# Performance work log

Hardware: AMD Instinct MI355X
Metric: run time of the kernel (lower is better)

The kernel has to match this reference:

```python
import jax, jax.numpy as jnp
import numpy as np

B, CIN, H, W = 4, 1024, 64, 64
PLANES = 256
K = 3
DIL = 2
PAD = DIL * (K - 1) // 2  # = 2
EPS = 1e-5


def setup_inputs() -> dict:
    key = jax.random.key(0)
    ks = jax.random.split(key, 16)
    d = {}
    d['x'] = jax.random.normal(ks[0], (B, CIN, H, W), dtype=jnp.float32)
    # conv1: 1x1, inplanes->planes, no bias
    d['w1'] = jax.random.normal(ks[1], (PLANES, CIN), dtype=jnp.float32) * 0.02
    d['gamma1'] = jnp.ones((PLANES,), jnp.float32)
    d['beta1'] = jnp.zeros((PLANES,), jnp.float32)
    d['mean1'] = jax.random.normal(ks[2], (PLANES,), dtype=jnp.float32) * 0.1
    d['var1'] = jax.random.uniform(ks[3], (PLANES,), minval=0.5, maxval=1.5, dtype=jnp.float32)
    # deform_offset: 3x3 conv planes->18, with bias
    d['woff'] = jax.random.normal(ks[4], (18, PLANES, K, K), dtype=jnp.float32) * 0.01
    d['boff'] = jnp.zeros((18,), jnp.float32)
    # conv2 (deformable): 3x3 planes->planes, with bias
    d['w2'] = jax.random.normal(ks[5], (PLANES, PLANES, K, K), dtype=jnp.float32) * 0.02
    d['bconv2'] = jnp.zeros((PLANES,), jnp.float32)
    d['gamma2'] = jnp.ones((PLANES,), jnp.float32)
    d['beta2'] = jnp.zeros((PLANES,), jnp.float32)
    d['mean2'] = jax.random.normal(ks[6], (PLANES,), dtype=jnp.float32) * 0.1
    d['var2'] = jax.random.uniform(ks[7], (PLANES,), minval=0.5, maxval=1.5, dtype=jnp.float32)
    # conv3: 1x1 planes->planes*4, no bias
    d['w3'] = jax.random.normal(ks[8], (PLANES * 4, PLANES), dtype=jnp.float32) * 0.02
    d['gamma3'] = jnp.ones((PLANES * 4,), jnp.float32)
    d['beta3'] = jnp.zeros((PLANES * 4,), jnp.float32)
    d['mean3'] = jax.random.normal(ks[9], (PLANES * 4,), dtype=jnp.float32) * 0.1
    d['var3'] = jax.random.uniform(ks[10], (PLANES * 4,), minval=0.5, maxval=1.5, dtype=jnp.float32)
    return d


def _bn(x, gamma, beta, mean, var):
    # inference-mode BatchNorm over channel dim (NCHW)
    inv = jax.lax.rsqrt(var + EPS)
    return (x - mean[:, None, None]) * (inv * gamma)[:, None, None] + beta[:, None, None]


def _deform_conv(x, offset, w, b):
    # x: [B,C,H,W]; offset: [B,18,H,W] ordered (dy,dx) per kernel tap; w: [O,C,3,3]
    Bn, C, Hh, Ww = x.shape
    off = offset.reshape(Bn, K * K, 2, Hh, Ww)
    off_y, off_x = off[:, :, 0], off[:, :, 1]          # [B,9,H,W]
    kk = jnp.arange(K * K)
    base_y = (kk // K) * DIL - PAD                      # [9]
    base_x = (kk % K) * DIL - PAD
    ys = jnp.arange(Hh, dtype=x.dtype)
    xs = jnp.arange(Ww, dtype=x.dtype)
    py = base_y.astype(x.dtype)[None, :, None, None] + ys[None, None, :, None] + off_y
    px = base_x.astype(x.dtype)[None, :, None, None] + xs[None, None, None, :] + off_x

    def sample_one(img, py1, px1):
        # img [C,H,W]; py1/px1 [9,H,W] -> [C,9,H,W] bilinear with zero padding
        y0 = jnp.floor(py1)
        x0 = jnp.floor(px1)
        wy = py1 - y0
        wx = px1 - x0

        def gather(yc, xc):
            yi = yc.astype(jnp.int32)
            xi = xc.astype(jnp.int32)
            valid = ((yi >= 0) & (yi < Hh) & (xi >= 0) & (xi < Ww)).astype(img.dtype)
            yi = jnp.clip(yi, 0, Hh - 1)
            xi = jnp.clip(xi, 0, Ww - 1)
            return img[:, yi, xi] * valid[None]

        v00 = gather(y0, x0)
        v01 = gather(y0, x0 + 1)
        v10 = gather(y0 + 1, x0)
        v11 = gather(y0 + 1, x0 + 1)
        return (v00 * ((1 - wy) * (1 - wx))[None] + v01 * ((1 - wy) * wx)[None]
                + v10 * (wy * (1 - wx))[None] + v11 * (wy * wx)[None])

    sampled = jax.vmap(sample_one)(x, py, px)           # [B,C,9,H,W]
    out = jnp.einsum('bckhw,ock->bohw', sampled, w.reshape(w.shape[0], C, K * K))
    return out + b[None, :, None, None]


def reference(x, w1, gamma1, beta1, mean1, var1, woff, boff, w2, bconv2,
              gamma2, beta2, mean2, var2, w3, gamma3, beta3, mean3, var3):
    residual = x
    out = jnp.einsum('bchw,oc->bohw', x, w1)            # conv1 1x1
    out = jax.nn.relu(_bn(out, gamma1, beta1, mean1, var1))
    offset = jax.lax.conv_general_dilated(
        out, woff, window_strides=(1, 1), padding=((PAD, PAD), (PAD, PAD)),
        rhs_dilation=(DIL, DIL), dimension_numbers=('NCHW', 'OIHW', 'NCHW'))
    offset = offset + boff[None, :, None, None]
    out = _deform_conv(out, offset, w2, bconv2)
    out = jax.nn.relu(_bn(out, gamma2, beta2, mean2, var2))
    out = jnp.einsum('bchw,oc->bohw', out, w3)          # conv3 1x1
    out = _bn(out, gamma3, beta3, mean3, var3)
    return jax.nn.relu(out + residual)
```

## Files before the change

### kernel.cpp

```cpp
#include <hip/hip_runtime.h>

#define EPS_BN 1e-5f

typedef __bf16 bf16x8 __attribute__((ext_vector_type(8)));
typedef float f32x4 __attribute__((ext_vector_type(4)));

__device__ __forceinline__ unsigned short f2bf(float f) {
  union { float f; unsigned u; } v; v.f = f;
  unsigned r = v.u + 0x7fffu + ((v.u >> 16) & 1u);
  return (unsigned short)(r >> 16);
}
__device__ __forceinline__ float bf2f(unsigned short h) {
  union { unsigned u; float f; } v; v.u = ((unsigned)h) << 16;
  return v.f;
}

__global__ __launch_bounds__(256) void prep_all(
    const float* __restrict__ w1, const float* __restrict__ w2, const float* __restrict__ woff,
    const float* __restrict__ w3,
    const float* g1, const float* b1, const float* m1, const float* v1,
    const float* g2, const float* b2, const float* m2, const float* v2, const float* bconv2,
    const float* g3, const float* b3, const float* m3, const float* v3,
    unsigned short* __restrict__ w1b, unsigned short* __restrict__ w2r,
    uint4* __restrict__ act1Pz, unsigned short* __restrict__ wob,
    unsigned short* __restrict__ w3b, float* __restrict__ shift3,
    float* s1, float* h1, float* s2, float* h2) {
  int bid = blockIdx.x, tid = threadIdx.x;
  if (bid < 1024) {
    int i = bid * 256 + tid;
    w1b[i] = f2bf(w1[i]);
  } else if (bid < 3328) {
    int i = (bid - 1024) * 256 + tid;
    int o = i / 2304, r = i % 2304;
    int kk = r / 256, c = r % 256;
    w2r[i] = f2bf(w2[(size_t)o * 2304 + c * 9 + kk]);
  } else if (bid < 5640) {
    int i = (bid - 3328) * 256 + tid;
    if (i < 591872) act1Pz[i] = uint4{0, 0, 0, 0};
  } else if (bid < 5928) {
    int i = (bid - 5640) * 256 + tid;
    int o = i / 2304, r = i % 2304;
    int kk = r / 256, c = r % 256;
    wob[i] = (o < 18) ? f2bf(woff[(size_t)o * 2304 + c * 9 + kk]) : (unsigned short)0;
  } else if (bid < 6952) {
    int i = (bid - 5928) * 256 + tid;
    int o = i >> 8;
    float sc = rsqrtf(v3[o] + EPS_BN) * g3[o];
    w3b[i] = f2bf(w3[i] * sc);
  } else if (bid < 6956) {
    int c = (bid - 6952) * 256 + tid;
    float sc = rsqrtf(v3[c] + EPS_BN) * g3[c];
    shift3[c] = b3[c] - m3[c] * sc;
  } else {
    int c = tid;
    float sc1 = rsqrtf(v1[c] + EPS_BN) * g1[c];
    s1[c] = sc1; h1[c] = b1[c] - m1[c] * sc1;
    float sc2 = rsqrtf(v2[c] + EPS_BN) * g2[c];
    s2[c] = sc2; h2[c] = b2[c] + (bconv2[c] - m2[c]) * sc2;
  }
}

__global__ __launch_bounds__(256) void transpose_x(const float* __restrict__ x,
                                                   unsigned short* __restrict__ xT) {
  __shared__ float t[32][33];
  int b = blockIdx.z;
  int p0 = blockIdx.x * 32, c0 = blockIdx.y * 32;
  int tx = threadIdx.x & 31, ty = threadIdx.x >> 5;
  const float* xb = x + (size_t)b * 1024 * 4096;
#pragma unroll
  for (int j = 0; j < 4; ++j) {
    int c = c0 + ty + j * 8;
    t[ty + j * 8][tx] = xb[(size_t)c * 4096 + p0 + tx];
  }
  __syncthreads();
  unsigned short* xTb = xT + (size_t)b * 4096 * 1024;
  int pl = threadIdx.x >> 3;
  int cl = (threadIdx.x & 7) * 4;
  float v0 = t[cl][pl], v1 = t[cl + 1][pl], v2 = t[cl + 2][pl], v3 = t[cl + 3][pl];
  uint2 pk;
  pk.x = (unsigned)f2bf(v0) | ((unsigned)f2bf(v1) << 16);
  pk.y = (unsigned)f2bf(v2) | ((unsigned)f2bf(v3) << 16);
  *(uint2*)(xTb + (size_t)(p0 + pl) * 1024 + c0 + cl) = pk;
}

__global__ __launch_bounds__(256) void gemm_split(
    const unsigned short* __restrict__ A, const unsigned short* __restrict__ Bm,
    unsigned short* __restrict__ part, int M, int N, int K, int KH) {
  __shared__ unsigned short sA[128 * 32];
  __shared__ unsigned short sB[128 * 32];
  __shared__ float tbuf[32 * 132];
  int tid = threadIdx.x, lane = tid & 63, wv = tid >> 6;
  int z = blockIdx.z;
  int m0 = blockIdx.y * 128, n0 = blockIdx.x * 128;
  f32x4 acc[4][4] = {};
  int rowA = tid >> 2;
  int kcol = (tid & 3) * 8;
  int wm = wv & 1, wn = wv >> 1;
  int lane15 = lane & 15, quad8 = (lane >> 4) * 8, quad = lane >> 4;
  int kend = z * KH + KH;

  for (int k0 = z * KH; k0 < kend; k0 += 32) {
    __syncthreads();
#pragma unroll
    for (int r = 0; r < 2; ++r) {
      const unsigned short* gp = A + (size_t)(m0 + r * 64 + rowA) * K + k0 + kcol;
      __builtin_amdgcn_global_load_lds((const __attribute__((address_space(1))) void*)gp,
                                       (__attribute__((address_space(3))) void*)&sA[r * 2048 + wv * 512],
                                       16, 0, 0);
    }
#pragma unroll
    for (int r = 0; r < 2; ++r) {
      const unsigned short* gp = Bm + (size_t)(n0 + r * 64 + rowA) * K + k0 + kcol;
      __builtin_amdgcn_global_load_lds((const __attribute__((address_space(1))) void*)gp,
                                       (__attribute__((address_space(3))) void*)&sB[r * 2048 + wv * 512],
                                       16, 0, 0);
    }
    __syncthreads();
    bf16x8 afr[4], bfr[4];
#pragma unroll
    for (int mi = 0; mi < 4; ++mi)
      afr[mi] = *(const bf16x8*)&sA[(wm * 64 + mi * 16 + lane15) * 32 + quad8];
#pragma unroll
    for (int ni = 0; ni < 4; ++ni)
      bfr[ni] = *(const bf16x8*)&sB[(wn * 64 + ni * 16 + lane15) * 32 + quad8];
#pragma unroll
    for (int mi = 0; mi < 4; ++mi)
#pragma unroll
      for (int ni = 0; ni < 4; ++ni)
        acc[mi][ni] = __builtin_amdgcn_mfma_f32_16x16x32_bf16(afr[mi], bfr[ni], acc[mi][ni], 0, 0, 0);
  }

  unsigned short* outH = part + (size_t)z * M * N;
  int trow = tid >> 3;
  int tcol16 = (tid & 7) * 16;
  int growBase = m0 + (trow >> 4) * 64 + (trow & 15);
#pragma unroll
  for (int mi = 0; mi < 4; ++mi) {
    __syncthreads();
#pragma unroll
    for (int ni = 0; ni < 4; ++ni)
#pragma unroll
      for (int reg = 0; reg < 4; ++reg)
        tbuf[(wm * 16 + quad * 4 + reg) * 132 + wn * 64 + ni * 16 + lane15] = acc[mi][ni][reg];
    __syncthreads();
    int gr = growBase + mi * 16;
    const float* lp = &tbuf[trow * 132 + tcol16];
    unsigned o[8];
#pragma unroll
    for (int j = 0; j < 8; ++j)
      o[j] = (unsigned)f2bf(lp[2 * j]) | ((unsigned)f2bf(lp[2 * j + 1]) << 16);
    unsigned short* op = outH + (size_t)gr * 256 + n0 + tcol16;
    *(uint4*)(op) = uint4{o[0], o[1], o[2], o[3]};
    *(uint4*)(op + 8) = uint4{o[4], o[5], o[6], o[7]};
  }
}

template <int NS, int PAD>
__global__ __launch_bounds__(256) void epi_bn(const unsigned short* __restrict__ part,
                                              const float* __restrict__ scale,
                                              const float* __restrict__ shift,
                                              unsigned short* __restrict__ outT,
                                              unsigned short* __restrict__ outP) {
  int gid = blockIdx.x * 256 + threadIdx.x;
  int row = gid >> 5, c0 = (gid & 31) * 8;
  float v[8] = {};
#pragma unroll
  for (int s = 0; s < NS; ++s) {
    uint4 q = *(const uint4*)(part + (size_t)s * 16384 * 256 + (size_t)row * 256 + c0);
    unsigned u[4] = {q.x, q.y, q.z, q.w};
#pragma unroll
    for (int j = 0; j < 4; ++j) {
      v[2 * j]     += bf2f((unsigned short)(u[j] & 0xffffu));
      v[2 * j + 1] += bf2f((unsigned short)(u[j] >> 16));
    }
  }
  float sc[8], sh[8];
  *(float4*)&sc[0] = *(const float4*)(scale + c0); *(float4*)&sc[4] = *(const float4*)(scale + c0 + 4);
  *(float4*)&sh[0] = *(const float4*)(shift + c0); *(float4*)&sh[4] = *(const float4*)(shift + c0 + 4);
  unsigned o[4];
#pragma unroll
  for (int j = 0; j < 4; ++j) {
    float lo = fmaxf(v[2 * j] * sc[2 * j] + sh[2 * j], 0.f);
    float hi = fmaxf(v[2 * j + 1] * sc[2 * j + 1] + sh[2 * j + 1], 0.f);
    o[j] = (unsigned)f2bf(lo) | ((unsigned)f2bf(hi) << 16);
  }
  uint4 pk{o[0], o[1], o[2], o[3]};
  *(uint4*)(outT + (size_t)row * 256 + c0) = pk;
  if constexpr (PAD) {
    int bb = row >> 12, p = row & 4095;
    *(uint4*)(outP + (((size_t)(bb * 68) + (p >> 6) + 2) * 68 + (p & 63) + 2) * 256 + c0) = pk;
  }
}

__global__ __launch_bounds__(256) void gemm_res(
    const unsigned short* __restrict__ A, const unsigned short* __restrict__ Bm,
    float* __restrict__ outp, const float* __restrict__ shift3,
    const float* __restrict__ resid, int M, int N, int K, long bStrideB, long bStrideOut) {
  __shared__ unsigned short sA[128 * 32];
  __shared__ unsigned short sB[128 * 32];
  __shared__ float tbuf[32 * 132];
  int tid = threadIdx.x, lane = tid & 63, wv = tid >> 6;
  int z = blockIdx.z;
  const unsigned short* Bz = Bm + (size_t)z * bStrideB;
  int m0 = blockIdx.y * 128, n0 = blockIdx.x * 128;
  f32x4 acc[4][4] = {};
  int rowA = tid >> 2;
  int kcol = (tid & 3) * 8;
  int wm = wv & 1, wn = wv >> 1;
  int lane15 = lane & 15, quad8 = (lane >> 4) * 8, quad = lane >> 4;

  for (int k0 = 0; k0 < K; k0 += 32) {
    __syncthreads();
#pragma unroll
    for (int r = 0; r < 2; ++r) {
      const unsigned short* gp = A + (size_t)(m0 + r * 64 + rowA) * K + k0 + kcol;
      __builtin_amdgcn_global_load_lds((const __attribute__((address_space(1))) void*)gp,
                                       (__attribute__((address_space(3))) void*)&sA[r * 2048 + wv * 512],
                                       16, 0, 0);
    }
#pragma unroll
    for (int r = 0; r < 2; ++r) {
      const unsigned short* gp = Bz + (size_t)(n0 + r * 64 + rowA) * K + k0 + kcol;
      __builtin_amdgcn_global_load_lds((const __attribute__((address_space(1))) void*)gp,
                                       (__attribute__((address_space(3))) void*)&sB[r * 2048 + wv * 512],
                                       16, 0, 0);
    }
    __syncthreads();
    bf16x8 afr[4], bfr[4];
#pragma unroll
    for (int mi = 0; mi < 4; ++mi)
      afr[mi] = *(const bf16x8*)&sA[(wm * 64 + mi * 16 + lane15) * 32 + quad8];
#pragma unroll
    for (int ni = 0; ni < 4; ++ni)
      bfr[ni] = *(const bf16x8*)&sB[(wn * 64 + ni * 16 + lane15) * 32 + quad8];
#pragma unroll
    for (int mi = 0; mi < 4; ++mi)
#pragma unroll
      for (int ni = 0; ni < 4; ++ni)
        acc[mi][ni] = __builtin_amdgcn_mfma_f32_16x16x32_bf16(afr[mi], bfr[ni], acc[mi][ni], 0, 0, 0);
  }

  float* outF = outp + (size_t)z * bStrideOut;
  const float* res = resid + (size_t)z * bStrideOut;
  int trow = tid >> 3;
  int tcol = (tid & 7) * 4;
  int growBase = m0 + (trow >> 4) * 64 + (trow & 15);
#pragma unroll
  for (int mi = 0; mi < 4; ++mi) {
    __syncthreads();
#pragma unroll
    for (int ni = 0; ni < 4; ++ni)
#pragma unroll
      for (int reg = 0; reg < 4; ++reg)
        tbuf[(wm * 16 + quad * 4 + reg) * 132 + wn * 64 + ni * 16 + lane15] = acc[mi][ni][reg];
    __syncthreads();
    int gr = growBase + mi * 16;
    float sh = shift3[gr];
    const float* rp = res + (size_t)gr * N + n0 + tcol;
    float* op = outF + (size_t)gr * N + n0 + tcol;
    const float* lp = &tbuf[trow * 132 + tcol];
#pragma unroll
    for (int j = 0; j < 4; ++j) {
      float4 rv = *(const float4*)(rp + j * 32);
      float4 lv = *(const float4*)(lp + j * 32);
      float4 ov;
      ov.x = fmaxf(lv.x + sh + rv.x, 0.f);
      ov.y = fmaxf(lv.y + sh + rv.y, 0.f);
      ov.z = fmaxf(lv.z + sh + rv.z, 0.f);
      ov.w = fmaxf(lv.w + sh + rv.w, 0.f);
      *(float4*)(op + j * 32) = ov;
    }
  }
}

__global__ __launch_bounds__(256) void off_gemm(const unsigned short* __restrict__ actP,
                                                const unsigned short* __restrict__ wob,
                                                const float* __restrict__ boff,
                                                float* __restrict__ offsP) {
  __shared__ unsigned short sA[64 * 64];
  __shared__ unsigned short sB[32 * 64];
  int tid = threadIdx.x, lane = tid & 63, wv = tid >> 6;
  int m0 = blockIdx.x * 64;
  int lane15 = lane & 15, quad8 = (lane >> 4) * 8;
  int rowA = tid >> 3;
  int kc = (tid & 7) * 8;

  const unsigned short* baseA[2];
#pragma unroll
  for (int r = 0; r < 2; ++r) {
    int row = m0 + r * 32 + rowA;
    int b = row >> 12, p = row & 4095;
    baseA[r] = actP + (((size_t)(b * 68) + (p >> 6) + 2) * 68 + (p & 63) + 2) * 256 + kc;
  }
  const unsigned short* baseB = wob + (size_t)rowA * 2304 + kc;

  f32x4 acc[2] = {};
  for (int kk = 0; kk < 9; ++kk) {
    int shift = ((kk / 3) * 2 - 2) * 68 + ((kk % 3) * 2 - 2);
#pragma unroll 1
    for (int c0 = 0; c0 < 256; c0 += 64) {
      __syncthreads();
#pragma unroll
      for (int r = 0; r < 2; ++r) {
        const unsigned short* gp = baseA[r] + (long)shift * 256 + c0;
        __builtin_amdgcn_global_load_lds((const __attribute__((address_space(1))) void*)gp,
                                         (__attribute__((address_space(3))) void*)&sA[r * 2048 + wv * 512],
                                         16, 0, 0);
      }
      {
        const unsigned short* gp = baseB + kk * 256 + c0;
        __builtin_amdgcn_global_load_lds((const __attribute__((address_space(1))) void*)gp,
                                         (__attribute__((address_space(3))) void*)&sB[wv * 512],
                                         16, 0, 0);
      }
      __syncthreads();
      bf16x8 afr[2], bfr[2][2];
#pragma unroll
      for (int kq = 0; kq < 2; ++kq) {
        afr[kq] = *(const bf16x8*)&sA[(wv * 16 + lane15) * 64 + kq * 32 + quad8];
#pragma unroll
        for (int ni = 0; ni < 2; ++ni)
          bfr[kq][ni] = *(const bf16x8*)&sB[(ni * 16 + lane15) * 64 + kq * 32 + quad8];
      }
#pragma unroll
      for (int kq = 0; kq < 2; ++kq)
#pragma unroll
        for (int ni = 0; ni < 2; ++ni)
          acc[ni] = __builtin_amdgcn_mfma_f32_16x16x32_bf16(afr[kq], bfr[kq][ni], acc[ni], 0, 0, 0);
    }
  }

#pragma unroll
  for (int ni = 0; ni < 2; ++ni) {
    int o = ni * 16 + lane15;
    if (o < 18) {
      float bo = boff[o];
#pragma unroll
      for (int reg = 0; reg < 4; ++reg) {
        int row = m0 + wv * 16 + (lane >> 4) * 4 + reg;
        offsP[(size_t)row * 18 + o] = acc[ni][reg] + bo;
      }
    }
  }
}

__global__ __launch_bounds__(256) void deform_sample(const unsigned short* __restrict__ act1T,
                                                     const float* __restrict__ offsP,
                                                     unsigned short* __restrict__ S) {
  int g = threadIdx.x >> 5, t = threadIdx.x & 31;
  int idx = blockIdx.x * 8 + g;
  int b = idx >> 12, p = idx & 4095;
  int h = p >> 6, w = p & 63;
  const unsigned short* actb = act1T + (size_t)b * 4096 * 256 + t * 8;
  unsigned short* Sp = S + (size_t)idx * 2304 + t * 8;
  float ov = (t < 18) ? offsP[(size_t)idx * 18 + t] : 0.f;
#pragma unroll
  for (int kk = 0; kk < 9; ++kk) {
    float offy = __shfl(ov, 2 * kk, 32);
    float offx = __shfl(ov, 2 * kk + 1, 32);
    float py = (float)(h + (kk / 3) * 2 - 2) + offy;
    float px = (float)(w + (kk % 3) * 2 - 2) + offx;
    float fy = floorf(py), fx = floorf(px);
    int y0 = (int)fy, x0 = (int)fx;
    float wy = py - fy, wx = px - fx;
    bool yv0 = (y0 >= 0 && y0 < 64), yv1 = (y0 >= -1 && y0 < 63);
    bool xv0 = (x0 >= 0 && x0 < 64), xv1 = (x0 >= -1 && x0 < 63);
    const unsigned short* cb = actb + (y0 * 64 + x0) * 256;
    uint4 q00{0,0,0,0}, q01{0,0,0,0}, q10{0,0,0,0}, q11{0,0,0,0};
    if (yv0 && xv0) q00 = *(const uint4*)(cb);
    if (yv0 && xv1) q01 = *(const uint4*)(cb + 256);
    if (yv1 && xv0) q10 = *(const uint4*)(cb + 64 * 256);
    if (yv1 && xv1) q11 = *(const uint4*)(cb + 64 * 256 + 256);
    float w00 = (1.f - wy) * (1.f - wx), w01 = (1.f - wy) * wx;
    float w10 = wy * (1.f - wx), w11 = wy * wx;
    unsigned u00[4] = {q00.x, q00.y, q00.z, q00.w};
    unsigned u01[4] = {q01.x, q01.y, q01.z, q01.w};
    unsigned u10[4] = {q10.x, q10.y, q10.z, q10.w};
    unsigned u11[4] = {q11.x, q11.y, q11.z, q11.w};
    unsigned out[4];
#pragma unroll
    for (int j = 0; j < 4; ++j) {
      float lo = bf2f((unsigned short)(u00[j] & 0xffffu)) * w00 +
                 bf2f((unsigned short)(u01[j] & 0xffffu)) * w01 +
                 bf2f((unsigned short)(u10[j] & 0xffffu)) * w10 +
                 bf2f((unsigned short)(u11[j] & 0xffffu)) * w11;
      float hi = bf2f((unsigned short)(u00[j] >> 16)) * w00 +
                 bf2f((unsigned short)(u01[j] >> 16)) * w01 +
                 bf2f((unsigned short)(u10[j] >> 16)) * w10 +
                 bf2f((unsigned short)(u11[j] >> 16)) * w11;
      out[j] = (unsigned)f2bf(lo) | ((unsigned)f2bf(hi) << 16);
    }
    *(uint4*)(Sp + kk * 256) = uint4{out[0], out[1], out[2], out[3]};
  }
}

extern "C" void kernel_launch(void* const* d_in, const int* in_sizes, int n_in,
                              void* d_out, int out_size, void* d_ws, size_t ws_size,
                              hipStream_t stream) {
  const float* x      = (const float*)d_in[0];
  const float* w1     = (const float*)d_in[1];
  const float* gamma1 = (const float*)d_in[2];
  const float* beta1  = (const float*)d_in[3];
  const float* mean1  = (const float*)d_in[4];
  const float* var1   = (const float*)d_in[5];
  const float* woff   = (const float*)d_in[6];
  const float* boff   = (const float*)d_in[7];
  const float* w2     = (const float*)d_in[8];
  const float* bconv2 = (const float*)d_in[9];
  const float* gamma2 = (const float*)d_in[10];
  const float* beta2  = (const float*)d_in[11];
  const float* mean2  = (const float*)d_in[12];
  const float* var2   = (const float*)d_in[13];
  const float* w3     = (const float*)d_in[14];
  const float* gamma3 = (const float*)d_in[15];
  const float* beta3  = (const float*)d_in[16];
  const float* mean3  = (const float*)d_in[17];
  const float* var3   = (const float*)d_in[18];

  char* ws = (char*)d_ws;
  unsigned short* xT    = (unsigned short*)(ws);
  unsigned short* act1T = (unsigned short*)(ws + 33554432);
  unsigned short* act2T = (unsigned short*)(ws + 41943040);
  unsigned short* S     = (unsigned short*)(ws + 50331648);
  float*          offs  = (float*)(ws + 125829120);
  unsigned short* w1b   = (unsigned short*)(ws + 127008768);
  unsigned short* w2r   = (unsigned short*)(ws + 127533056);
  unsigned short* w3b   = (unsigned short*)(ws + 128712704);
  float*          bnS1  = (float*)(ws + 129236992);
  float*          bnH1  = (float*)(ws + 129238016);
  float*          bnS2  = (float*)(ws + 129239040);
  float*          bnH2  = (float*)(ws + 129240064);
  float*          shift3= (float*)(ws + 129241088);
  unsigned short* act1P = S;
  unsigned short* part1 = (unsigned short*)(ws + 62914560);
  unsigned short* part2 = (unsigned short*)ws;
  unsigned short* wob   = act2T;

  prep_all<<<6957, 256, 0, stream>>>(w1, w2, woff, w3,
                                     gamma1, beta1, mean1, var1,
                                     gamma2, beta2, mean2, var2, bconv2,
                                     gamma3, beta3, mean3, var3,
                                     w1b, w2r, (uint4*)act1P, wob, w3b, shift3,
                                     bnS1, bnH1, bnS2, bnH2);
  transpose_x<<<dim3(128, 32, 4), 256, 0, stream>>>(x, xT);

  gemm_split<<<dim3(2, 128, 2), 256, 0, stream>>>(xT, w1b, part1, 16384, 256, 1024, 512);
  epi_bn<2, 1><<<2048, 256, 0, stream>>>(part1, bnS1, bnH1, act1T, act1P);

  off_gemm<<<256, 256, 0, stream>>>(act1P, wob, boff, offs);
  deform_sample<<<dim3(2048), 256, 0, stream>>>(act1T, offs, S);

  gemm_split<<<dim3(2, 128, 2), 256, 0, stream>>>(S, w2r, part2, 16384, 256, 2304, 1152);
  epi_bn<2, 0><<<2048, 256, 0, stream>>>(part2, bnS2, bnH2, act2T, nullptr);

  gemm_res<<<dim3(32, 8, 4), 256, 0, stream>>>(w3b, act2T, (float*)d_out, shift3, x,
                                               1024, 4096, 256, 4096L * 256, 4194304L);
}
```

Measured before the change: 299.9 us.

## Double-buffer LDS in GEMM kernels and raise split-K to four

Converts the K loops of gemm_split, gemm_res and off_gemm to a two-stage LDS ping-pong. The global-to-LDS load for the next K slice is issued before the MFMA work on the current one, which also removes one barrier per iteration. The epilogue staging buffer now aliases the operand buffers in LDS. Separately, the conv1 and deform GEMMs use split-K of 4 instead of 2 to launch more blocks, at the cost of writing and reducing twice as many bf16 partial buffers and of more workspace.

```diff
diff --git a/kernel.cpp b/kernel.cpp
--- a/kernel.cpp
+++ b/kernel.cpp
@@ -86,9 +86,12 @@
 __global__ __launch_bounds__(256) void gemm_split(
     const unsigned short* __restrict__ A, const unsigned short* __restrict__ Bm,
     unsigned short* __restrict__ part, int M, int N, int K, int KH) {
-  __shared__ unsigned short sA[128 * 32];
-  __shared__ unsigned short sB[128 * 32];
-  __shared__ float tbuf[32 * 132];
+  __shared__ __align__(16) char smem[32768];
+  unsigned short* sA0 = (unsigned short*)smem;
+  unsigned short* sB0 = (unsigned short*)(smem + 8192);
+  unsigned short* sA1 = (unsigned short*)(smem + 16384);
+  unsigned short* sB1 = (unsigned short*)(smem + 24576);
+  float* tbuf = (float*)smem;
   int tid = threadIdx.x, lane = tid & 63, wv = tid >> 6;
   int z = blockIdx.z;
   int m0 = blockIdx.y * 128, n0 = blockIdx.x * 128;
@@ -97,38 +100,49 @@
   int kcol = (tid & 3) * 8;
   int wm = wv & 1, wn = wv >> 1;
   int lane15 = lane & 15, quad8 = (lane >> 4) * 8, quad = lane >> 4;
-  int kend = z * KH + KH;
-
-  for (int k0 = z * KH; k0 < kend; k0 += 32) {
-    __syncthreads();
-#pragma unroll
-    for (int r = 0; r < 2; ++r) {
-      const unsigned short* gp = A + (size_t)(m0 + r * 64 + rowA) * K + k0 + kcol;
-      __builtin_amdgcn_global_load_lds((const __attribute__((address_space(1))) void*)gp,
-                                       (__attribute__((address_space(3))) void*)&sA[r * 2048 + wv * 512],
-                                       16, 0, 0);
-    }
-#pragma unroll
-    for (int r = 0; r < 2; ++r) {
-      const unsigned short* gp = Bm + (size_t)(n0 + r * 64 + rowA) * K + k0 + kcol;
-      __builtin_amdgcn_global_load_lds((const __attribute__((address_space(1))) void*)gp,
-                                       (__attribute__((address_space(3))) void*)&sB[r * 2048 + wv * 512],
-                                       16, 0, 0);
-    }
-    __syncthreads();
-    bf16x8 afr[4], bfr[4];
-#pragma unroll
-    for (int mi = 0; mi < 4; ++mi)
-      afr[mi] = *(const bf16x8*)&sA[(wm * 64 + mi * 16 + lane15) * 32 + quad8];
-#pragma unroll
-    for (int ni = 0; ni < 4; ++ni)
-      bfr[ni] = *(const bf16x8*)&sB[(wn * 64 + ni * 16 + lane15) * 32 + quad8];
-#pragma unroll
-    for (int mi = 0; mi < 4; ++mi)
-#pragma unroll
-      for (int ni = 0; ni < 4; ++ni)
-        acc[mi][ni] = __builtin_amdgcn_mfma_f32_16x16x32_bf16(afr[mi], bfr[ni], acc[mi][ni], 0, 0, 0);
-  }
+
+#define GS_STAGE(dA, dB, K0)                                                              \
+  {                                                                                       \
+    int k0_ = (K0);                                                                       \
+    _Pragma("unroll") for (int r = 0; r < 2; ++r) {                                       \
+      const unsigned short* gp = A + (size_t)(m0 + r * 64 + rowA) * K + k0_ + kcol;       \
+      __builtin_amdgcn_global_load_lds((const __attribute__((address_space(1))) void*)gp, \
+          (__attribute__((address_space(3))) void*)&(dA)[r * 2048 + wv * 512], 16, 0, 0); \
+    }                                                                                     \
+    _Pragma("unroll") for (int r = 0; r < 2; ++r) {                                       \
+      const unsigned short* gp = Bm + (size_t)(n0 + r * 64 + rowA) * K + k0_ + kcol;      \
+      __builtin_amdgcn_global_load_lds((const __attribute__((address_space(1))) void*)gp, \
+          (__attribute__((address_space(3))) void*)&(dB)[r * 2048 + wv * 512], 16, 0, 0); \
+    }                                                                                     \
+  }
+
+#define GS_COMPUTE(dA, dB)                                                                \
+  {                                                                                       \
+    bf16x8 afr[4], bfr[4];                                                                \
+    _Pragma("unroll") for (int mi = 0; mi < 4; ++mi)                                      \
+      afr[mi] = *(const bf16x8*)&(dA)[(wm * 64 + mi * 16 + lane15) * 32 + quad8];         \
+    _Pragma("unroll") for (int ni = 0; ni < 4; ++ni)                                      \
+      bfr[ni] = *(const bf16x8*)&(dB)[(wn * 64 + ni * 16 + lane15) * 32 + quad8];         \
+    _Pragma("unroll") for (int mi = 0; mi < 4; ++mi)                                      \
+      _Pragma("unroll") for (int ni = 0; ni < 4; ++ni)                                    \
+        acc[mi][ni] =                                                                     \
+            __builtin_amdgcn_mfma_f32_16x16x32_bf16(afr[mi], bfr[ni], acc[mi][ni], 0, 0, 0); \
+  }
+
+  int kbase = z * KH;
+  int nst = KH >> 5;
+  GS_STAGE(sA0, sB0, kbase);
+  __syncthreads();
+  for (int t = 0; t < nst; t += 2) {
+    GS_STAGE(sA1, sB1, kbase + (t + 1) * 32);
+    GS_COMPUTE(sA0, sB0);
+    __syncthreads();
+    if (t + 2 < nst) GS_STAGE(sA0, sB0, kbase + (t + 2) * 32);
+    GS_COMPUTE(sA1, sB1);
+    __syncthreads();
+  }
+#undef GS_STAGE
+#undef GS_COMPUTE
 
   unsigned short* outH = part + (size_t)z * M * N;
   int trow = tid >> 3;
@@ -196,9 +210,12 @@
     const unsigned short* __restrict__ A, const unsigned short* __restrict__ Bm,
     float* __restrict__ outp, const float* __restrict__ shift3,
     const float* __restrict__ resid, int M, int N, int K, long bStrideB, long bStrideOut) {
-  __shared__ unsigned short sA[128 * 32];
-  __shared__ unsigned short sB[128 * 32];
-  __shared__ float tbuf[32 * 132];
+  __shared__ __align__(16) char smem[32768];
+  unsigned short* sA0 = (unsigned short*)smem;
+  unsigned short* sB0 = (unsigned short*)(smem + 8192);
+  unsigned short* sA1 = (unsigned short*)(smem + 16384);
+  unsigned short* sB1 = (unsigned short*)(smem + 24576);
+  float* tbuf = (float*)smem;
   int tid = threadIdx.x, lane = tid & 63, wv = tid >> 6;
   int z = blockIdx.z;
   const unsigned short* Bz = Bm + (size_t)z * bStrideB;
@@ -209,36 +226,47 @@
   int wm = wv & 1, wn = wv >> 1;
   int lane15 = lane & 15, quad8 = (lane >> 4) * 8, quad = lane >> 4;
 
-  for (int k0 = 0; k0 < K; k0 += 32) {
-    __syncthreads();
-#pragma unroll
-    for (int r = 0; r < 2; ++r) {
-      const unsigned short* gp = A + (size_t)(m0 + r * 64 + rowA) * K + k0 + kcol;
-      __builtin_amdgcn_global_load_lds((const __attribute__((address_space(1))) void*)gp,
-                                       (__attribute__((address_space(3))) void*)&sA[r * 2048 + wv * 512],
-                                       16, 0, 0);
-    }
-#pragma unroll
-    for (int r = 0; r < 2; ++r) {
-      const unsigned short* gp = Bz + (size_t)(n0 + r * 64 + rowA) * K + k0 + kcol;
-      __builtin_amdgcn_global_load_lds((const __attribute__((address_space(1))) void*)gp,
-                                       (__attribute__((address_space(3))) void*)&sB[r * 2048 + wv * 512],
-                                       16, 0, 0);
-    }
-    __syncthreads();
-    bf16x8 afr[4], bfr[4];
-#pragma unroll
-    for (int mi = 0; mi < 4; ++mi)
-      afr[mi] = *(const bf16x8*)&sA[(wm * 64 + mi * 16 + lane15) * 32 + quad8];
-#pragma unroll
-    for (int ni = 0; ni < 4; ++ni)
-      bfr[ni] = *(const bf16x8*)&sB[(wn * 64 + ni * 16 + lane15) * 32 + quad8];
-#pragma unroll
-    for (int mi = 0; mi < 4; ++mi)
-#pragma unroll
-      for (int ni = 0; ni < 4; ++ni)
-        acc[mi][ni] = __builtin_amdgcn_mfma_f32_16x16x32_bf16(afr[mi], bfr[ni], acc[mi][ni], 0, 0, 0);
-  }
+#define GR_STAGE(dA, dB, K0)                                                              \
+  {                                                                                       \
+    int k0_ = (K0);                                                                       \
+    _Pragma("unroll") for (int r = 0; r < 2; ++r) {                                       \
+      const unsigned short* gp = A + (size_t)(m0 + r * 64 + rowA) * K + k0_ + kcol;       \
+      __builtin_amdgcn_global_load_lds((const __attribute__((address_space(1))) void*)gp, \
+          (__attribute__((address_space(3))) void*)&(dA)[r * 2048 + wv * 512], 16, 0, 0); \
+    }                                                                                     \
+    _Pragma("unroll") for (int r = 0; r < 2; ++r) {                                       \
+      const unsigned short* gp = Bz + (size_t)(n0 + r * 64 + rowA) * K + k0_ + kcol;      \
+      __builtin_amdgcn_global_load_lds((const __attribute__((address_space(1))) void*)gp, \
+          (__attribute__((address_space(3))) void*)&(dB)[r * 2048 + wv * 512], 16, 0, 0); \
+    }                                                                                     \
+  }
+
+#define GR_COMPUTE(dA, dB)                                                                \
+  {                                                                                       \
+    bf16x8 afr[4], bfr[4];                                                                \
+    _Pragma("unroll") for (int mi = 0; mi < 4; ++mi)                                      \
+      afr[mi] = *(const bf16x8*)&(dA)[(wm * 64 + mi * 16 + lane15) * 32 + quad8];         \
+    _Pragma("unroll") for (int ni = 0; ni < 4; ++ni)                                      \
+      bfr[ni] = *(const bf16x8*)&(dB)[(wn * 64 + ni * 16 + lane15) * 32 + quad8];         \
+    _Pragma("unroll") for (int mi = 0; mi < 4; ++mi)                                      \
+      _Pragma("unroll") for (int ni = 0; ni < 4; ++ni)                                    \
+        acc[mi][ni] =                                                                     \
+            __builtin_amdgcn_mfma_f32_16x16x32_bf16(afr[mi], bfr[ni], acc[mi][ni], 0, 0, 0); \
+  }
+
+  int nst = K >> 5;
+  GR_STAGE(sA0, sB0, 0);
+  __syncthreads();
+  for (int t = 0; t < nst; t += 2) {
+    GR_STAGE(sA1, sB1, (t + 1) * 32);
+    GR_COMPUTE(sA0, sB0);
+    __syncthreads();
+    if (t + 2 < nst) GR_STAGE(sA0, sB0, (t + 2) * 32);
+    GR_COMPUTE(sA1, sB1);
+    __syncthreads();
+  }
+#undef GR_STAGE
+#undef GR_COMPUTE
 
   float* outF = outp + (size_t)z * bStrideOut;
   const float* res = resid + (size_t)z * bStrideOut;
@@ -277,8 +305,11 @@
                                                 const unsigned short* __restrict__ wob,
                                                 const float* __restrict__ boff,
                                                 float* __restrict__ offsP) {
-  __shared__ unsigned short sA[64 * 64];
-  __shared__ unsigned short sB[32 * 64];
+  __shared__ __align__(16) char smem[24576];
+  unsigned short* sA0 = (unsigned short*)smem;
+  unsigned short* sB0 = (unsigned short*)(smem + 8192);
+  unsigned short* sA1 = (unsigned short*)(smem + 12288);
+  unsigned short* sB1 = (unsigned short*)(smem + 20480);
   int tid = threadIdx.x, lane = tid & 63, wv = tid >> 6;
   int m0 = blockIdx.x * 64;
   int lane15 = lane & 15, quad8 = (lane >> 4) * 8;
@@ -295,40 +326,48 @@
   const unsigned short* baseB = wob + (size_t)rowA * 2304 + kc;
 
   f32x4 acc[2] = {};
-  for (int kk = 0; kk < 9; ++kk) {
-    int shift = ((kk / 3) * 2 - 2) * 68 + ((kk % 3) * 2 - 2);
-#pragma unroll 1
-    for (int c0 = 0; c0 < 256; c0 += 64) {
-      __syncthreads();
-#pragma unroll
-      for (int r = 0; r < 2; ++r) {
-        const unsigned short* gp = baseA[r] + (long)shift * 256 + c0;
-        __builtin_amdgcn_global_load_lds((const __attribute__((address_space(1))) void*)gp,
-                                         (__attribute__((address_space(3))) void*)&sA[r * 2048 + wv * 512],
-                                         16, 0, 0);
-      }
-      {
-        const unsigned short* gp = baseB + kk * 256 + c0;
-        __builtin_amdgcn_global_load_lds((const __attribute__((address_space(1))) void*)gp,
-                                         (__attribute__((address_space(3))) void*)&sB[wv * 512],
-                                         16, 0, 0);
-      }
-      __syncthreads();
-      bf16x8 afr[2], bfr[2][2];
-#pragma unroll
-      for (int kq = 0; kq < 2; ++kq) {
-        afr[kq] = *(const bf16x8*)&sA[(wv * 16 + lane15) * 64 + kq * 32 + quad8];
-#pragma unroll
-        for (int ni = 0; ni < 2; ++ni)
-          bfr[kq][ni] = *(const bf16x8*)&sB[(ni * 16 + lane15) * 64 + kq * 32 + quad8];
-      }
-#pragma unroll
-      for (int kq = 0; kq < 2; ++kq)
-#pragma unroll
-        for (int ni = 0; ni < 2; ++ni)
-          acc[ni] = __builtin_amdgcn_mfma_f32_16x16x32_bf16(afr[kq], bfr[kq][ni], acc[ni], 0, 0, 0);
-    }
-  }
+
+#define OG_STAGE(dA, dB, S)                                                               \
+  {                                                                                       \
+    int s_ = (S); int kk_ = s_ >> 2; int c0_ = (s_ & 3) * 64;                             \
+    long shift_ = (long)(((kk_ / 3) * 2 - 2) * 68 + ((kk_ % 3) * 2 - 2));                 \
+    _Pragma("unroll") for (int r = 0; r < 2; ++r) {                                       \
+      const unsigned short* gp = baseA[r] + shift_ * 256 + c0_;                           \
+      __builtin_amdgcn_global_load_lds((const __attribute__((address_space(1))) void*)gp, \
+          (__attribute__((address_space(3))) void*)&(dA)[r * 2048 + wv * 512], 16, 0, 0); \
+    }                                                                                     \
+    {                                                                                     \
+      const unsigned short* gp = baseB + kk_ * 256 + c0_;                                 \
+      __builtin_amdgcn_global_load_lds((const __attribute__((address_space(1))) void*)gp, \
+          (__attribute__((address_space(3))) void*)&(dB)[wv * 512], 16, 0, 0);            \
+    }                                                                                     \
+  }
+
+#define OG_COMPUTE(dA, dB)                                                                \
+  {                                                                                       \
+    bf16x8 afr[2], bfr[2][2];                                                             \
+    _Pragma("unroll") for (int kq = 0; kq < 2; ++kq) {                                    \
+      afr[kq] = *(const bf16x8*)&(dA)[(wv * 16 + lane15) * 64 + kq * 32 + quad8];         \
+      _Pragma("unroll") for (int ni = 0; ni < 2; ++ni)                                    \
+        bfr[kq][ni] = *(const bf16x8*)&(dB)[(ni * 16 + lane15) * 64 + kq * 32 + quad8];   \
+    }                                                                                     \
+    _Pragma("unroll") for (int kq = 0; kq < 2; ++kq)                                      \
+      _Pragma("unroll") for (int ni = 0; ni < 2; ++ni)                                    \
+        acc[ni] = __builtin_amdgcn_mfma_f32_16x16x32_bf16(afr[kq], bfr[kq][ni], acc[ni], 0, 0, 0); \
+  }
+
+  OG_STAGE(sA0, sB0, 0);
+  __syncthreads();
+  for (int s = 0; s < 36; s += 2) {
+    OG_STAGE(sA1, sB1, s + 1);
+    OG_COMPUTE(sA0, sB0);
+    __syncthreads();
+    if (s + 2 < 36) OG_STAGE(sA0, sB0, s + 2);
+    OG_COMPUTE(sA1, sB1);
+    __syncthreads();
+  }
+#undef OG_STAGE
+#undef OG_COMPUTE
 
 #pragma unroll
   for (int ni = 0; ni < 2; ++ni) {
@@ -444,14 +483,14 @@
                                      bnS1, bnH1, bnS2, bnH2);
   transpose_x<<<dim3(128, 32, 4), 256, 0, stream>>>(x, xT);
 
-  gemm_split<<<dim3(2, 128, 2), 256, 0, stream>>>(xT, w1b, part1, 16384, 256, 1024, 512);
-  epi_bn<2, 1><<<2048, 256, 0, stream>>>(part1, bnS1, bnH1, act1T, act1P);
+  gemm_split<<<dim3(2, 128, 4), 256, 0, stream>>>(xT, w1b, part1, 16384, 256, 1024, 256);
+  epi_bn<4, 1><<<2048, 256, 0, stream>>>(part1, bnS1, bnH1, act1T, act1P);
 
   off_gemm<<<256, 256, 0, stream>>>(act1P, wob, boff, offs);
   deform_sample<<<dim3(2048), 256, 0, stream>>>(act1T, offs, S);
 
-  gemm_split<<<dim3(2, 128, 2), 256, 0, stream>>>(S, w2r, part2, 16384, 256, 2304, 1152);
-  epi_bn<2, 0><<<2048, 256, 0, stream>>>(part2, bnS2, bnH2, act2T, nullptr);
+  gemm_split<<<dim3(2, 128, 4), 256, 0, stream>>>(S, w2r, part2, 16384, 256, 2304, 576);
+  epi_bn<4, 0><<<2048, 256, 0, stream>>>(part2, bnS2, bnH2, act2T, nullptr);
 
   gemm_res<<<dim3(32, 8, 4), 256, 0, stream>>>(w3b, act2T, (float*)d_out, shift3, x,
                                                1024, 4096, 256, 4096L * 256, 4194304L);
```

New measurement: 307.5 us. 1.03x slower.
